# Kernel optimization log

Hardware: AMD Instinct MI355X
Metric: run time of the kernel (lower is better)

The kernel has to match this reference:

```python
import jax, jax.numpy as jnp
import numpy as np

N = 50000      # nodes per type
E = 800000     # edges per relation
F_IN = 256
HID = 256
OUT = 128


def _edges(k):
    e = jax.random.randint(k, (2, E), 0, N)
    src, dst = e[0], e[1]
    # ensure no pre-existing self loops (PyG adds remaining self loops itself)
    src = jnp.where(src == dst, (src + 1) % N, src)
    return jnp.stack([src, dst]).astype(jnp.int64)


def _w(k, i, o):
    return (jax.random.normal(k, (i, o), jnp.float32) / np.float32(np.sqrt(i)))


def setup_inputs() -> dict:
    key = jax.random.key(0)
    ks = jax.random.split(key, 40)
    inp = {
        'x_lnc_jac': jax.random.normal(ks[0], (N, F_IN), jnp.float32),
        'x_prot_jac': jax.random.normal(ks[1], (N, F_IN), jnp.float32),
        'x_lnc_blast': jax.random.normal(ks[2], (N, F_IN), jnp.float32),
        'x_prot_blast': jax.random.normal(ks[3], (N, F_IN), jnp.float32),
        'edge_jac_lnc': _edges(ks[4]),
        'edge_jac_prot': _edges(ks[5]),
        'edge_blast_lnc': _edges(ks[6]),
        'edge_blast_prot': _edges(ks[7]),
        # jaccard view GCN weights (layer1: F_IN->HID, layer2: HID->OUT)
        'W_j1_lnc': _w(ks[8], F_IN, HID), 'b_j1_lnc': jnp.zeros((HID,), jnp.float32),
        'W_j1_prot': _w(ks[9], F_IN, HID), 'b_j1_prot': jnp.zeros((HID,), jnp.float32),
        'W_j2_lnc': _w(ks[10], HID, OUT), 'b_j2_lnc': jnp.zeros((OUT,), jnp.float32),
        'W_j2_prot': _w(ks[11], HID, OUT), 'b_j2_prot': jnp.zeros((OUT,), jnp.float32),
        # blast view GCN weights
        'W_b1_lnc': _w(ks[12], F_IN, HID), 'b_b1_lnc': jnp.zeros((HID,), jnp.float32),
        'W_b1_prot': _w(ks[13], F_IN, HID), 'b_b1_prot': jnp.zeros((HID,), jnp.float32),
        'W_b2_lnc': _w(ks[14], HID, OUT), 'b_b2_lnc': jnp.zeros((OUT,), jnp.float32),
        'W_b2_prot': _w(ks[15], HID, OUT), 'b_b2_prot': jnp.zeros((OUT,), jnp.float32),
        # residual linears
        'W_res_lnc': _w(ks[16], F_IN, OUT), 'b_res_lnc': jnp.zeros((OUT,), jnp.float32),
        'W_res_prot': _w(ks[17], F_IN, OUT), 'b_res_prot': jnp.zeros((OUT,), jnp.float32),
    }
    return inp


def _gcn(x, edge_index, W, b):
    # PyG GCNConv: add self loops, sym-normalize, transform, scatter-add, +bias
    src, dst = edge_index[0], edge_index[1]
    n = x.shape[0]
    xw = x @ W                                             # [N, F_out]
    ones = jnp.ones((src.shape[0],), xw.dtype)
    deg = jax.ops.segment_sum(ones, dst, num_segments=n) + 1.0  # in-deg + self loop
    dinv = jax.lax.rsqrt(deg)
    coef = (dinv[src] * dinv[dst])[:, None]
    agg = jax.ops.segment_sum(xw[src] * coef, dst, num_segments=n)
    return agg + xw / deg[:, None] + b                      # self-loop norm = 1/deg


def _lrelu(x):
    return jnp.where(x >= 0, x, 0.2 * x)


def reference(x_lnc_jac, x_prot_jac, x_lnc_blast, x_prot_blast,
              edge_jac_lnc, edge_jac_prot, edge_blast_lnc, edge_blast_prot,
              W_j1_lnc, b_j1_lnc, W_j1_prot, b_j1_prot,
              W_j2_lnc, b_j2_lnc, W_j2_prot, b_j2_prot,
              W_b1_lnc, b_b1_lnc, W_b1_prot, b_b1_prot,
              W_b2_lnc, b_b2_lnc, W_b2_prot, b_b2_prot,
              W_res_lnc, b_res_lnc, W_res_prot, b_res_prot):
    # jaccard view: 2 GCN layers per node type (HeteroConv mean over a single
    # relation per destination type is identity)
    h = _lrelu(_gcn(x_lnc_jac, edge_jac_lnc, W_j1_lnc, b_j1_lnc))
    jl = _lrelu(_gcn(h, edge_jac_lnc, W_j2_lnc, b_j2_lnc))
    h = _lrelu(_gcn(x_prot_jac, edge_jac_prot, W_j1_prot, b_j1_prot))
    jp = _lrelu(_gcn(h, edge_jac_prot, W_j2_prot, b_j2_prot))
    # blast view
    h = _lrelu(_gcn(x_lnc_blast, edge_blast_lnc, W_b1_lnc, b_b1_lnc))
    bl = _lrelu(_gcn(h, edge_blast_lnc, W_b2_lnc, b_b2_lnc))
    h = _lrelu(_gcn(x_prot_blast, edge_blast_prot, W_b1_prot, b_b1_prot))
    bp = _lrelu(_gcn(h, edge_blast_prot, W_b2_prot, b_b2_prot))
    # fuse views + residual from the ORIGINAL jaccard features
    comb_l = (jl + bl) * 0.5 + (x_lnc_jac @ W_res_lnc + b_res_lnc)
    comb_p = (jp + bp) * 0.5 + (x_prot_jac @ W_res_prot + b_res_prot)
    return (comb_l, comb_p, jl, jp, bl, bp)
```

## Files before the change

### kernel.cpp

```cpp
#include <hip/hip_runtime.h>
#include <cstddef>

#define NN 50000
#define NE 800000

typedef __bf16 bf16x8 __attribute__((ext_vector_type(8)));
typedef float floatx4 __attribute__((ext_vector_type(4)));

__device__ __forceinline__ float bflo2f(unsigned int u) {
    union { unsigned int u; float f; } v; v.u = u << 16; return v.f;
}
__device__ __forceinline__ float bfhi2f(unsigned int u) {
    union { unsigned int u; float f; } v; v.u = u & 0xffff0000u; return v.f;
}
__device__ __forceinline__ unsigned short f2bf(float f) {
    union { float f; unsigned int u; } v; v.f = f;
    unsigned int u = v.u;
    unsigned int r = u + 0x7fffu + ((u >> 16) & 1u);
    return (unsigned short)(r >> 16);
}


#define NBUK 98
#define BSH  9
#define ACH  4096
#define BKCAP 12288

__global__ void k_binit2(int* __restrict__ bfill) {
    int i = blockIdx.x * blockDim.x + threadIdx.x;
    if (i < 4 * 128) bfill[i] = (i & 127) * BKCAP;
}

__global__ __launch_bounds__(256) void k_bucketA(
        const int* __restrict__ e0, const int* __restrict__ e1,
        const int* __restrict__ e2, const int* __restrict__ e3,
        int* __restrict__ bfill, uint2* __restrict__ pairbuf) {
    __shared__ int lcnt[128];
    __shared__ int s1[128];
    __shared__ int lbase[128];
    __shared__ int lfil[128];
    __shared__ int gbase[128];
    __shared__ uint2 sbuf[ACH];

    const int* es[4] = {e0, e1, e2, e3};
    const int r = blockIdx.y;
    const int tid = threadIdx.x;
    const int* src = es[r];
    const int* dst = es[r] + NE;
    const int lo = blockIdx.x * ACH;
    int hi = lo + ACH; if (hi > NE) hi = NE;
    const int cnt = hi - lo;

    if (tid < 128) lcnt[tid] = 0;
    __syncthreads();

    for (int i = lo + tid; i < hi; i += 256)
        atomicAdd(&lcnt[dst[i] >> BSH], 1);
    __syncthreads();

    if (tid < 128) s1[tid] = lcnt[tid];
    __syncthreads();
    for (int o = 1; o < 128; o <<= 1) {
        int x = (tid < 128 && tid >= o) ? s1[tid - o] : 0;
        __syncthreads();
        if (tid < 128) s1[tid] += x;
        __syncthreads();
    }
    if (tid < 128) {
        int eb = s1[tid] - lcnt[tid];
        lbase[tid] = eb;
        lfil[tid] = eb;
    }
    __syncthreads();

    for (int i = lo + tid; i < hi; i += 256) {
        int d = dst[i];
        int b = d >> BSH;
        int p = atomicAdd(&lfil[b], 1);
        uint2 v; v.x = (unsigned int)src[i]; v.y = (unsigned int)d;
        sbuf[p] = v;
    }
    __syncthreads();

    if (tid < 128 && lcnt[tid] > 0)
        gbase[tid] = atomicAdd(&bfill[r * 128 + tid], lcnt[tid]);
    __syncthreads();

    uint2* pout = pairbuf + (size_t)r * (128 * (size_t)BKCAP);
    for (int i = tid; i < cnt; i += 256) {
        int loB = 0, hiB = 128;
        while (hiB - loB > 1) {
            int m = (loB + hiB) >> 1;
            if (lbase[m] <= i) loB = m; else hiB = m;
        }
        pout[(size_t)gbase[loB] + (i - lbase[loB])] = sbuf[i];
    }
}

__global__ void k_bscan(const int* __restrict__ bfill, int* __restrict__ bbase,
                        int* __restrict__ rowptr) {
    __shared__ int sd[128];
    int t = threadIdx.x;
    for (int r = 0; r < 4; r++) {
        int c = bfill[r * 128 + t] - t * BKCAP;
        sd[t] = c; __syncthreads();
        for (int o = 1; o < 128; o <<= 1) {
            int x = (t >= o) ? sd[t - o] : 0; __syncthreads();
            sd[t] += x; __syncthreads();
        }
        bbase[r * 128 + t] = sd[t] - c;
        __syncthreads();
    }
    if (t == 0)
        for (int r = 0; r < 4; r++) rowptr[r * (NN + 1) + NN] = NE;
}

__global__ __launch_bounds__(256) void k_bucketB(
        const uint2* __restrict__ pairbuf, const int* __restrict__ bfill,
        const int* __restrict__ bbase, int* __restrict__ rowptr,
        float* __restrict__ dinv, int* __restrict__ csr_src) {
    __shared__ int csrimg[BKCAP];
    __shared__ int lcnt[512];
    __shared__ int lcur[512];

    const int r = blockIdx.y;
    const int b = blockIdx.x;
    const int tid = threadIdx.x;
    const int node_lo = b << BSH;
    int node_hi = node_lo + 512; if (node_hi > NN) node_hi = NN;
    const int nr = node_hi - node_lo;

    const int pbase = b * BKCAP;
    int cnt = bfill[r * 128 + b] - pbase;
    if (cnt > BKCAP) cnt = BKCAP;
    const int seg0 = bbase[r * 128 + b];

    lcnt[tid] = 0; lcnt[tid + 256] = 0;
    __syncthreads();

    const uint2* pb = pairbuf + (size_t)r * (128 * (size_t)BKCAP) + pbase;
    for (int i = tid; i < cnt; i += 256) {
        int li = (int)pb[i].y - node_lo;
        if (li >= 0 && li < 512) atomicAdd(&lcnt[li], 1);
    }
    __syncthreads();
    lcur[tid] = lcnt[tid]; lcur[tid + 256] = lcnt[tid + 256];
    __syncthreads();
    for (int o = 1; o < 512; o <<= 1) {
        int a0 = (tid >= o) ? lcnt[tid - o] : 0;
        int a1 = (tid + 256 >= o) ? lcnt[tid + 256 - o] : 0;
        __syncthreads();
        lcnt[tid] += a0; lcnt[tid + 256] += a1;
        __syncthreads();
    }
#pragma unroll
    for (int jj = 0; jj < 2; jj++) {
        int j = tid + jj * 256;
        int c = lcur[j];
        int excl = lcnt[j] - c;
        if (j < nr) {
            rowptr[r * (NN + 1) + node_lo + j] = seg0 + excl;
            dinv[r * NN + node_lo + j] = rsqrtf((float)(c + 1));
        }
        lcur[j] = excl;
    }
    __syncthreads();
    for (int i = tid; i < cnt; i += 256) {
        uint2 p = pb[i];
        int li = (int)p.y - node_lo;
        if (li >= 0 && li < 512) {
            int s = atomicAdd(&lcur[li], 1);
            if (s >= 0 && s < BKCAP) csrimg[s] = (int)p.x;
        }
    }
    __syncthreads();
    int* co = csr_src + (size_t)r * NE + seg0;
    for (int k = tid; k < cnt; k += 256) co[k] = csrimg[k];
}


struct WTArgs {
    const float* W[10];
    unsigned short* Wt[10];
    int M[10];
};

__global__ void k_wT_all(WTArgs a) {
    int g = blockIdx.y;
    int M = a.M[g];
    int total = 256 * M;
    int i = blockIdx.x * blockDim.x + threadIdx.x;
    if (i < total) {
        int m = i >> 8, k = i & 255;
        a.Wt[g][i] = f2bf(a.W[g][(size_t)k * M + m]);
    }
}

#define GB_BM 128
#define GB_BN 128
#define GB_BK 32

template <bool AF32>
__global__ __launch_bounds__(256) void k_gemm(
        const void* __restrict__ Aptr, const unsigned short* __restrict__ Bt,
        int nrows, int K, int ncols,
        unsigned short* __restrict__ outBf, float* __restrict__ outF,
        const float* __restrict__ add0, const float* __restrict__ add1,
        const float* __restrict__ bias, int mode) {
    __shared__ __align__(16) unsigned short As[GB_BM][GB_BK];
    __shared__ __align__(16) unsigned short Bs[GB_BN][GB_BK];
    const int tid = threadIdx.x;
    const int lane = tid & 63;
    const int wid = tid >> 6;
    const int wm = (wid >> 1) * 64;
    const int wn = (wid & 1) * 64;
    const int row0 = blockIdx.x * GB_BM;
    const int col0 = blockIdx.y * GB_BN;
    const int lrow = lane & 15;
    const int lquad = lane >> 4;

    floatx4 acc[4][4];
#pragma unroll
    for (int i = 0; i < 4; i++)
#pragma unroll
        for (int j = 0; j < 4; j++) acc[i][j] = (floatx4){0.f, 0.f, 0.f, 0.f};

    for (int k0 = 0; k0 < K; k0 += GB_BK) {
#pragma unroll
        for (int t = 0; t < 2; t++) {
            int c = tid + t * 256;
            int r = c >> 2;
            int co = (c & 3) * 8;
            int gr = row0 + r; if (gr >= nrows) gr = nrows - 1;
            if constexpr (AF32) {
                const float* pa = (const float*)Aptr + (size_t)gr * K + k0 + co;
                float4 v0 = *(const float4*)pa;
                float4 v1 = *(const float4*)(pa + 4);
                uint4 o;
                o.x = (unsigned int)f2bf(v0.x) | ((unsigned int)f2bf(v0.y) << 16);
                o.y = (unsigned int)f2bf(v0.z) | ((unsigned int)f2bf(v0.w) << 16);
                o.z = (unsigned int)f2bf(v1.x) | ((unsigned int)f2bf(v1.y) << 16);
                o.w = (unsigned int)f2bf(v1.z) | ((unsigned int)f2bf(v1.w) << 16);
                *(uint4*)&As[r][co] = o;
            } else {
                *(uint4*)&As[r][co] =
                    *(const uint4*)((const unsigned short*)Aptr + (size_t)gr * K + k0 + co);
            }
            int gc = col0 + r;
            *(uint4*)&Bs[r][co] = *(const uint4*)(Bt + (size_t)gc * K + k0 + co);
        }
        __syncthreads();
        bf16x8 af[4], bfr[4];
#pragma unroll
        for (int i = 0; i < 4; i++) af[i] = *(const bf16x8*)&As[wm + 16 * i + lrow][lquad * 8];
#pragma unroll
        for (int j = 0; j < 4; j++) bfr[j] = *(const bf16x8*)&Bs[wn + 16 * j + lrow][lquad * 8];
#pragma unroll
        for (int i = 0; i < 4; i++)
#pragma unroll
            for (int j = 0; j < 4; j++)
                acc[i][j] = __builtin_amdgcn_mfma_f32_16x16x32_bf16(af[i], bfr[j], acc[i][j], 0, 0, 0);
        __syncthreads();
    }

#pragma unroll
    for (int i = 0; i < 4; i++) {
#pragma unroll
        for (int j = 0; j < 4; j++) {
            int col = col0 + wn + 16 * j + lrow;
#pragma unroll
            for (int r = 0; r < 4; r++) {
                int row = row0 + wm + 16 * i + lquad * 4 + r;
                if (row < nrows) {
                    float v = acc[i][j][r];
                    size_t idx = (size_t)row * ncols + col;
                    if (mode == 0) {
                        outBf[idx] = f2bf(v);
                    } else {
                        outF[idx] = v + bias[col] + 0.5f * (add0[idx] + add1[idx]);
                    }
                }
            }
        }
    }
}


__device__ __forceinline__ void ldrow4(const unsigned short* p, float* o) {
    uint2 r = *(const uint2*)p;
    o[0] = bflo2f(r.x & 0xffffu); o[1] = bfhi2f(r.x);
    o[2] = bflo2f(r.y & 0xffffu); o[3] = bfhi2f(r.y);
}
__device__ __forceinline__ void ldrow2(const unsigned short* p, float* o) {
    unsigned int r = *(const unsigned int*)p;
    o[0] = bflo2f(r & 0xffffu); o[1] = bfhi2f(r);
}

template <int NC>
__global__ __launch_bounds__(256) void k_aggregate(
        const unsigned short* __restrict__ xw,
        const int* __restrict__ rowptr,
        const int* __restrict__ cs,
        const float* __restrict__ dinv,
        const float* __restrict__ bias,
        unsigned short* __restrict__ outB,
        float* __restrict__ outF, int mode, int n) {
    constexpr int F = NC * 64;
    const int lane = threadIdx.x & 63;
    const int wid = blockIdx.x * (blockDim.x >> 6) + (threadIdx.x >> 6);
    const int nw = gridDim.x * (blockDim.x >> 6);
    const int fb = lane * NC;

    float bv[NC];
#pragma unroll
    for (int c = 0; c < NC; c++) bv[c] = bias[fb + c];

    for (int i = wid; i < n; i += nw) {
        float di = dinv[i];
        float acc[NC];
        {
            float rv[NC];
            if constexpr (NC == 4) ldrow4(xw + (size_t)i * F + fb, rv);
            else                   ldrow2(xw + (size_t)i * F + fb, rv);
#pragma unroll
            for (int c = 0; c < NC; c++) acc[c] = di * rv[c];
        }
        int e0 = rowptr[i], e1 = rowptr[i + 1];
        int j = e0;
        for (; j + 3 < e1; j += 4) {
            int s0 = cs[j], s1 = cs[j + 1], s2 = cs[j + 2], s3 = cs[j + 3];
            float c0 = dinv[s0], c1 = dinv[s1], c2 = dinv[s2], c3 = dinv[s3];
            float r0[NC], r1[NC], r2[NC], r3[NC];
            if constexpr (NC == 4) {
                ldrow4(xw + (size_t)s0 * F + fb, r0);
                ldrow4(xw + (size_t)s1 * F + fb, r1);
                ldrow4(xw + (size_t)s2 * F + fb, r2);
                ldrow4(xw + (size_t)s3 * F + fb, r3);
            } else {
                ldrow2(xw + (size_t)s0 * F + fb, r0);
                ldrow2(xw + (size_t)s1 * F + fb, r1);
                ldrow2(xw + (size_t)s2 * F + fb, r2);
                ldrow2(xw + (size_t)s3 * F + fb, r3);
            }
#pragma unroll
            for (int c = 0; c < NC; c++)
                acc[c] += c0 * r0[c] + c1 * r1[c] + c2 * r2[c] + c3 * r3[c];
        }
        for (; j < e1; j++) {
            int s = cs[j];
            float cf = dinv[s];
            float rv[NC];
            if constexpr (NC == 4) ldrow4(xw + (size_t)s * F + fb, rv);
            else                   ldrow2(xw + (size_t)s * F + fb, rv);
#pragma unroll
            for (int c = 0; c < NC; c++) acc[c] += cf * rv[c];
        }
#pragma unroll
        for (int c = 0; c < NC; c++) {
            float v = di * acc[c] + bv[c];
            acc[c] = v >= 0.f ? v : 0.2f * v;
        }
        if (mode == 0) {
            if constexpr (NC == 4) {
                uint2 o;
                o.x = (unsigned int)f2bf(acc[0]) | ((unsigned int)f2bf(acc[1]) << 16);
                o.y = (unsigned int)f2bf(acc[2]) | ((unsigned int)f2bf(acc[3]) << 16);
                *(uint2*)(outB + (size_t)i * F + fb) = o;
            } else {
                *(unsigned int*)(outB + (size_t)i * F + fb) =
                    (unsigned int)f2bf(acc[0]) | ((unsigned int)f2bf(acc[1]) << 16);
            }
        } else {
            if constexpr (NC == 4) {
                float4 o = {acc[0], acc[1], acc[2], acc[3]};
                *(float4*)(outF + (size_t)i * F + fb) = o;
            } else {
                float2 o = {acc[0], acc[1]};
                *(float2*)(outF + (size_t)i * F + fb) = o;
            }
        }
    }
}


static inline size_t alignup(size_t x) { return (x + 255) & ~(size_t)255; }

extern "C" void kernel_launch(void* const* d_in, const int* in_sizes, int n_in,
                              void* d_out, int out_size, void* d_ws, size_t ws_size,
                              hipStream_t stream) {
    const float* x[4]  = {(const float*)d_in[0], (const float*)d_in[1],
                          (const float*)d_in[2], (const float*)d_in[3]};
    const int* ed[4]   = {(const int*)d_in[4], (const int*)d_in[5],
                          (const int*)d_in[6], (const int*)d_in[7]};
    const float* W1[4] = {(const float*)d_in[8],  (const float*)d_in[10],
                          (const float*)d_in[16], (const float*)d_in[18]};
    const float* b1[4] = {(const float*)d_in[9],  (const float*)d_in[11],
                          (const float*)d_in[17], (const float*)d_in[19]};
    const float* W2[4] = {(const float*)d_in[12], (const float*)d_in[14],
                          (const float*)d_in[20], (const float*)d_in[22]};
    const float* b2[4] = {(const float*)d_in[13], (const float*)d_in[15],
                          (const float*)d_in[21], (const float*)d_in[23]};
    const float* Wr[2] = {(const float*)d_in[24], (const float*)d_in[26]};
    const float* br[2] = {(const float*)d_in[25], (const float*)d_in[27]};

    float* out = (float*)d_out;
    const size_t S = (size_t)NN * 128;

    char* w = (char*)d_ws;
    int*   rowptr  = (int*)w;                w += alignup((size_t)4 * (NN + 1) * 4);
    float* dinv    = (float*)w;              w += alignup((size_t)4 * NN * 4);
    int*   bfill   = (int*)w;                w += alignup((size_t)4 * 128 * 4);
    int*   bbase   = (int*)w;                w += alignup((size_t)4 * 128 * 4);
    int*   csr_src = (int*)w;                w += alignup((size_t)4 * NE * 4);
    unsigned short* xw1 = (unsigned short*)w;  w += alignup((size_t)NN * 256 * 2);
    unsigned short* hbf = (unsigned short*)w;  w += alignup((size_t)NN * 256 * 2);
    unsigned short* xw2 = (unsigned short*)w;  w += alignup((size_t)NN * 128 * 2);
    unsigned short* WtA = (unsigned short*)w;  w += alignup((size_t)(4 * 256 * 256 + 6 * 128 * 256) * 2);

    uint2* pairbuf = (uint2*)xw1;

    unsigned short* Wt1[4], * Wt2[4], * Wtr[2];
    {
        unsigned short* p = WtA;
        for (int i = 0; i < 4; i++) { Wt1[i] = p; p += 256 * 256; }
        for (int i = 0; i < 4; i++) { Wt2[i] = p; p += 128 * 256; }
        for (int i = 0; i < 2; i++) { Wtr[i] = p; p += 128 * 256; }
    }

    k_binit2<<<2, 256, 0, stream>>>(bfill);
    k_bucketA<<<dim3((NE + ACH - 1) / ACH, 4), 256, 0, stream>>>(
            ed[0], ed[1], ed[2], ed[3], bfill, pairbuf);
    k_bscan<<<1, 128, 0, stream>>>(bfill, bbase, rowptr);
    k_bucketB<<<dim3(NBUK, 4), 256, 0, stream>>>(pairbuf, bfill, bbase,
            rowptr, dinv, csr_src);

    {
        WTArgs a;
        for (int i = 0; i < 4; i++) { a.W[i] = W1[i];     a.Wt[i] = Wt1[i];     a.M[i] = 256; }
        for (int i = 0; i < 4; i++) { a.W[4 + i] = W2[i]; a.Wt[4 + i] = Wt2[i]; a.M[4 + i] = 128; }
        for (int i = 0; i < 2; i++) { a.W[8 + i] = Wr[i]; a.Wt[8 + i] = Wtr[i]; a.M[8 + i] = 128; }
        k_wT_all<<<dim3(256, 10), 256, 0, stream>>>(a);
    }

    const int gx = (NN + GB_BM - 1) / GB_BM;
    for (int p = 0; p < 4; p++) {
        const int* rp = rowptr + p * (NN + 1);
        const int* cs = csr_src + (size_t)p * NE;
        const float* dv = dinv + (size_t)p * NN;

        k_gemm<true><<<dim3(gx, 2), 256, 0, stream>>>(x[p], Wt1[p], NN, 256, 256,
                xw1, nullptr, nullptr, nullptr, nullptr, 0);
        k_aggregate<4><<<2048, 256, 0, stream>>>(xw1, rp, cs, dv, b1[p],
                hbf, nullptr, 0, NN);
        k_gemm<false><<<dim3(gx, 1), 256, 0, stream>>>(hbf, Wt2[p], NN, 256, 128,
                xw2, nullptr, nullptr, nullptr, nullptr, 0);
        k_aggregate<2><<<2048, 256, 0, stream>>>(xw2, rp, cs, dv, b2[p],
                nullptr, out + (2 + p) * S, 1, NN);
    }

    for (int t = 0; t < 2; t++) {
        const float* a0 = out + (2 + t) * S;
        const float* a1 = out + (4 + t) * S;
        k_gemm<true><<<dim3(gx, 1), 256, 0, stream>>>(x[t], Wtr[t], NN, 256, 128,
                nullptr, out + t * S, a0, a1, br[t], 1);
    }
}
```

Measured before the change: 1.057 ms.

## Batch the four relation pipelines into grouped GEMM and aggregate launches

Replaces the per-relation sequence of sixteen GEMM/aggregate launches plus two residual GEMMs with five grouped launches. The relation index comes from an extra grid dimension, and pointer tables are passed in argument structs. Intermediate buffers are widened to hold all four relations at once. This removes launch gaps and the tail under-utilisation of small per-relation kernels, at the cost of about four times the workspace for intermediates and a larger working set that no longer fits in cache between stages.

```diff
diff --git a/kernel.cpp b/kernel.cpp
--- a/kernel.cpp
+++ b/kernel.cpp
@@ -200,15 +200,24 @@
 #define GB_BN 128
 #define GB_BK 32
 
+struct GemmArgs {
+    const void* A[4];
+    const unsigned short* Bt[4];
+    unsigned short* outBf[4];
+    float* outF[4];
+    const float* add0[4];
+    const float* add1[4];
+    const float* bias[4];
+};
+
 template <bool AF32>
-__global__ __launch_bounds__(256) void k_gemm(
-        const void* __restrict__ Aptr, const unsigned short* __restrict__ Bt,
-        int nrows, int K, int ncols,
-        unsigned short* __restrict__ outBf, float* __restrict__ outF,
-        const float* __restrict__ add0, const float* __restrict__ add1,
-        const float* __restrict__ bias, int mode) {
+__global__ __launch_bounds__(256) void k_gemmB(
+        GemmArgs g, int nrows, int K, int ncols, int mode) {
     __shared__ __align__(16) unsigned short As[GB_BM][GB_BK];
     __shared__ __align__(16) unsigned short Bs[GB_BN][GB_BK];
+    const int z = blockIdx.z;
+    const void* __restrict__ Aptr = g.A[z];
+    const unsigned short* __restrict__ Bt = g.Bt[z];
     const int tid = threadIdx.x;
     const int lane = tid & 63;
     const int wid = tid >> 6;
@@ -263,6 +272,11 @@
         __syncthreads();
     }
 
+    unsigned short* outBf = g.outBf[z];
+    float* outF = g.outF[z];
+    const float* add0 = g.add0[z];
+    const float* add1 = g.add1[z];
+    const float* bias = g.bias[z];
 #pragma unroll
     for (int i = 0; i < 4; i++) {
 #pragma unroll
@@ -296,16 +310,28 @@
     o[0] = bflo2f(r & 0xffffu); o[1] = bfhi2f(r);
 }
 
+struct AggArgs {
+    const unsigned short* xw[4];
+    const int* rp[4];
+    const int* cs[4];
+    const float* dv[4];
+    const float* bias[4];
+    unsigned short* outB[4];
+    float* outF[4];
+};
+
 template <int NC>
-__global__ __launch_bounds__(256) void k_aggregate(
-        const unsigned short* __restrict__ xw,
-        const int* __restrict__ rowptr,
-        const int* __restrict__ cs,
-        const float* __restrict__ dinv,
-        const float* __restrict__ bias,
-        unsigned short* __restrict__ outB,
-        float* __restrict__ outF, int mode, int n) {
+__global__ __launch_bounds__(256) void k_aggB(AggArgs a, int mode, int n) {
     constexpr int F = NC * 64;
+    const int rel = blockIdx.y;
+    const unsigned short* __restrict__ xw = a.xw[rel];
+    const int* __restrict__ rowptr = a.rp[rel];
+    const int* __restrict__ cs = a.cs[rel];
+    const float* __restrict__ dinv = a.dv[rel];
+    const float* __restrict__ bias = a.bias[rel];
+    unsigned short* __restrict__ outB = a.outB[rel];
+    float* __restrict__ outF = a.outF[rel];
+
     const int lane = threadIdx.x & 63;
     const int wid = blockIdx.x * (blockDim.x >> 6) + (threadIdx.x >> 6);
     const int nw = gridDim.x * (blockDim.x >> 6);
@@ -412,10 +438,10 @@
     int*   bfill   = (int*)w;                w += alignup((size_t)4 * 128 * 4);
     int*   bbase   = (int*)w;                w += alignup((size_t)4 * 128 * 4);
     int*   csr_src = (int*)w;                w += alignup((size_t)4 * NE * 4);
-    unsigned short* xw1 = (unsigned short*)w;  w += alignup((size_t)NN * 256 * 2);
-    unsigned short* hbf = (unsigned short*)w;  w += alignup((size_t)NN * 256 * 2);
-    unsigned short* xw2 = (unsigned short*)w;  w += alignup((size_t)NN * 128 * 2);
     unsigned short* WtA = (unsigned short*)w;  w += alignup((size_t)(4 * 256 * 256 + 6 * 128 * 256) * 2);
+    unsigned short* xw1 = (unsigned short*)w;  w += alignup((size_t)4 * NN * 256 * 2);
+    unsigned short* hbf = (unsigned short*)w;  w += alignup((size_t)4 * NN * 256 * 2);
+    unsigned short* xw2 = (unsigned short*)w;  w += alignup((size_t)4 * NN * 128 * 2);
 
     uint2* pairbuf = (uint2*)xw1;
 
@@ -425,6 +451,12 @@
         for (int i = 0; i < 4; i++) { Wt1[i] = p; p += 256 * 256; }
         for (int i = 0; i < 4; i++) { Wt2[i] = p; p += 128 * 256; }
         for (int i = 0; i < 2; i++) { Wtr[i] = p; p += 128 * 256; }
+    }
+    unsigned short* xw1r[4], * hbfr[4], * xw2r[4];
+    for (int i = 0; i < 4; i++) {
+        xw1r[i] = xw1 + (size_t)i * NN * 256;
+        hbfr[i] = hbf + (size_t)i * NN * 256;
+        xw2r[i] = xw2 + (size_t)i * NN * 128;
     }
 
     k_binit2<<<2, 256, 0, stream>>>(bfill);
@@ -443,25 +475,50 @@
     }
 
     const int gx = (NN + GB_BM - 1) / GB_BM;
-    for (int p = 0; p < 4; p++) {
-        const int* rp = rowptr + p * (NN + 1);
-        const int* cs = csr_src + (size_t)p * NE;
-        const float* dv = dinv + (size_t)p * NN;
-
-        k_gemm<true><<<dim3(gx, 2), 256, 0, stream>>>(x[p], Wt1[p], NN, 256, 256,
-                xw1, nullptr, nullptr, nullptr, nullptr, 0);
-        k_aggregate<4><<<2048, 256, 0, stream>>>(xw1, rp, cs, dv, b1[p],
-                hbf, nullptr, 0, NN);
-        k_gemm<false><<<dim3(gx, 1), 256, 0, stream>>>(hbf, Wt2[p], NN, 256, 128,
-                xw2, nullptr, nullptr, nullptr, nullptr, 0);
-        k_aggregate<2><<<2048, 256, 0, stream>>>(xw2, rp, cs, dv, b2[p],
-                nullptr, out + (2 + p) * S, 1, NN);
-    }
-
-    for (int t = 0; t < 2; t++) {
-        const float* a0 = out + (2 + t) * S;
-        const float* a1 = out + (4 + t) * S;
-        k_gemm<true><<<dim3(gx, 1), 256, 0, stream>>>(x[t], Wtr[t], NN, 256, 128,
-                nullptr, out + t * S, a0, a1, br[t], 1);
-    }
-}
+
+    {
+        GemmArgs g{};
+        for (int p = 0; p < 4; p++) {
+            g.A[p] = x[p]; g.Bt[p] = Wt1[p]; g.outBf[p] = xw1r[p];
+            g.outF[p] = nullptr; g.add0[p] = nullptr; g.add1[p] = nullptr; g.bias[p] = nullptr;
+        }
+        k_gemmB<true><<<dim3(gx, 2, 4), 256, 0, stream>>>(g, NN, 256, 256, 0);
+    }
+    {
+        AggArgs a{};
+        for (int p = 0; p < 4; p++) {
+            a.xw[p] = xw1r[p]; a.rp[p] = rowptr + p * (NN + 1);
+            a.cs[p] = csr_src + (size_t)p * NE; a.dv[p] = dinv + (size_t)p * NN;
+            a.bias[p] = b1[p]; a.outB[p] = hbfr[p]; a.outF[p] = nullptr;
+        }
+        k_aggB<4><<<dim3(2048, 4), 256, 0, stream>>>(a, 0, NN);
+    }
+    {
+        GemmArgs g{};
+        for (int p = 0; p < 4; p++) {
+            g.A[p] = hbfr[p]; g.Bt[p] = Wt2[p]; g.outBf[p] = xw2r[p];
+            g.outF[p] = nullptr; g.add0[p] = nullptr; g.add1[p] = nullptr; g.bias[p] = nullptr;
+        }
+        k_gemmB<false><<<dim3(gx, 1, 4), 256, 0, stream>>>(g, NN, 256, 128, 0);
+    }
+    {
+        AggArgs a{};
+        for (int p = 0; p < 4; p++) {
+            a.xw[p] = xw2r[p]; a.rp[p] = rowptr + p * (NN + 1);
+            a.cs[p] = csr_src + (size_t)p * NE; a.dv[p] = dinv + (size_t)p * NN;
+            a.bias[p] = b2[p]; a.outB[p] = nullptr; a.outF[p] = out + (2 + p) * S;
+        }
+        k_aggB<2><<<dim3(2048, 4), 256, 0, stream>>>(a, 1, NN);
+    }
+    {
+        GemmArgs g{};
+        for (int t = 0; t < 2; t++) {
+            g.A[t] = x[t]; g.Bt[t] = Wtr[t]; g.outBf[t] = nullptr;
+            g.outF[t] = out + t * S;
+            g.add0[t] = out + (2 + t) * S;
+            g.add1[t] = out + (4 + t) * S;
+            g.bias[t] = br[t];
+        }
+        k_gemmB<true><<<dim3(gx, 1, 2), 256, 0, stream>>>(g, NN, 256, 128, 1);
+    }
+}
```

New measurement: 994.5 us. 1.06x faster.
